# Performance work log

Hardware: AMD Instinct MI355X
Metric: run time of the kernel (lower is better)

Reference implementation:

```python
import jax, jax.numpy as jnp
import numpy as np

HEADS = 32
DK = 32            # att_size = hidden // heads
CUT = 15.5         # tot_dis[cur_layer=0] + 0.5
NEG = -1e8
LN_EPS = 1e-5


def layernorm(x, g, b):
    m = jnp.mean(x, axis=-1, keepdims=True)
    v = jnp.mean((x - m) ** 2, axis=-1, keepdims=True)
    return (x - m) / jnp.sqrt(v + LN_EPS) * g + b


def setup_inputs() -> dict:
    key = jax.random.key(0)
    ks = jax.random.split(key, 12)
    B, S, H, F = 8, 513, 1024, 4096
    N = S - 1
    def nrm(k, shape, scale=0.02):
        return jax.random.normal(k, shape, jnp.float32) * scale
    x = jax.random.normal(ks[0], (B, S, H), jnp.float32)
    attn_bias = jax.random.normal(ks[1], (B, HEADS, S, S), jnp.float32)
    rel_pos = jax.random.randint(ks[2], (B, N, N), 0, 16, jnp.int32)
    rel_emb = nrm(ks[3], (512, HEADS)).at[0].set(0.0)  # padding_idx=0
    Wq = nrm(ks[4], (H, H)); bq = jnp.zeros((H,), jnp.float32)
    Wk = nrm(ks[5], (H, H)); bk = jnp.zeros((H,), jnp.float32)
    Wv = nrm(ks[6], (H, H)); bv = jnp.zeros((H,), jnp.float32)
    Wo = nrm(ks[7], (H, H)); bo = jnp.zeros((H,), jnp.float32)
    W1 = nrm(ks[8], (H, F)); b1 = jnp.zeros((F,), jnp.float32)
    W2 = nrm(ks[9], (F, H)); b2 = jnp.zeros((H,), jnp.float32)
    ln1_g = jnp.ones((H,), jnp.float32); ln1_b = jnp.zeros((H,), jnp.float32)
    ln2_g = jnp.ones((H,), jnp.float32); ln2_b = jnp.zeros((H,), jnp.float32)
    return dict(x=x, attn_bias=attn_bias, rel_emb=rel_emb,
                Wq=Wq, bq=bq, Wk=Wk, bk=bk, Wv=Wv, bv=bv, Wo=Wo, bo=bo,
                W1=W1, b1=b1, W2=W2, b2=b2,
                ln1_g=ln1_g, ln1_b=ln1_b, ln2_g=ln2_g, ln2_b=ln2_b,
                rel_pos=rel_pos)


def reference(x, attn_bias, rel_emb, Wq, bq, Wk, bk, Wv, bv, Wo, bo,
              W1, b1, W2, b2, ln1_g, ln1_b, ln2_g, ln2_b, rel_pos):
    B, S, H = x.shape
    # rel-pos bias: embed [B,N,N] -> [B,N,N,heads] -> [B,heads,N,N]
    rpb = jnp.transpose(rel_emb[rel_pos], (0, 3, 1, 2))
    inner = attn_bias[:, :, 1:, 1:] + rpb
    # per-head mask flag: keep if within cutoff distance OR already -inf-masked
    flags = (rel_pos[:, None, :, :] <= CUT) | (inner < NEG)
    ab = attn_bias.at[:, :, 1:, 1:].set(inner * flags)
    # attention
    y = layernorm(x, ln1_g, ln1_b)
    scale = DK ** -0.5
    q = (y @ Wq + bq).reshape(B, S, HEADS, DK) * scale
    k = (y @ Wk + bk).reshape(B, S, HEADS, DK)
    v = (y @ Wv + bv).reshape(B, S, HEADS, DK)
    scores = jnp.einsum('bqhd,bkhd->bhqk', q, k) + ab
    attn = jax.nn.softmax(scores, axis=-1)
    o = jnp.einsum('bhqk,bkhd->bqhd', attn, v).reshape(B, S, H)
    x = x + (o @ Wo + bo)
    # FFN
    y = layernorm(x, ln2_g, ln2_b)
    y = jax.nn.gelu(y @ W1 + b1, approximate=False) @ W2 + b2
    return x + y
```

## Files before the change

kernel.cpp:

```cpp
#include <hip/hip_runtime.h>
#include <hip/hip_bf16.h>
#include <math.h>

typedef __attribute__((ext_vector_type(8))) short short8;
typedef __attribute__((ext_vector_type(4))) float f32x4;
typedef unsigned short u16;
typedef unsigned int u32;

#define SQ 513
#define MPAD 4224
#define MV 4104
#define NHEADS 32
#define DKH 32

static __device__ inline u16 f2bf(float f) {
  u32 u = __builtin_bit_cast(u32, f);
  u = (u + 0x7fffu + ((u >> 16) & 1u)) >> 16;
  return (u16)u;
}

static __device__ inline void gld16(const void* g, void* l) {
  __builtin_amdgcn_global_load_lds((__attribute__((address_space(1))) void*)g,
                                   (__attribute__((address_space(3))) void*)l,
                                   16, 0, 0);
}

static __device__ inline float gelu_f(float x) {
  return 0.5f * x * (1.f + erff(x * 0.70710678118654752f));
}

__global__ __launch_bounds__(256) void transpose_cast_k(const float* __restrict__ in,
    u16* __restrict__ out, int K, int N, float scale)
{
  __shared__ float t[32][33];
  int n0 = blockIdx.x * 32, k0 = blockIdx.y * 32;
  int tx = threadIdx.x & 31, ty = threadIdx.x >> 5;
#pragma unroll
  for (int i = 0; i < 32; i += 8)
    t[ty + i][tx] = in[(size_t)(k0 + ty + i) * N + n0 + tx];
  __syncthreads();
#pragma unroll
  for (int i = 0; i < 32; i += 8)
    out[(size_t)(n0 + ty + i) * K + k0 + tx] = f2bf(t[tx][ty + i] * scale);
}

__global__ __launch_bounds__(256) void prep_bias_k(const float* __restrict__ bq,
    const float* __restrict__ bk, const float* __restrict__ bv,
    float* __restrict__ out, float scale)
{
  int i = blockIdx.x * 256 + threadIdx.x;
  float v = (i < 1024) ? bq[i] * scale : ((i < 2048) ? bk[i - 1024] : bv[i - 2048]);
  out[i] = v;
}

__global__ __launch_bounds__(256) void ln_k(const float* __restrict__ in,
    const float* __restrict__ g, const float* __restrict__ b,
    u16* __restrict__ out)
{
  int row = blockIdx.x;
  float4 v = ((const float4*)(in + (size_t)row * 1024))[threadIdx.x];
  float s = v.x + v.y + v.z + v.w;
  float s2 = v.x * v.x + v.y * v.y + v.z * v.z + v.w * v.w;
#pragma unroll
  for (int d = 32; d; d >>= 1) { s += __shfl_xor(s, d, 64); s2 += __shfl_xor(s2, d, 64); }
  __shared__ float ps[4], ps2[4];
  int w = threadIdx.x >> 6;
  if ((threadIdx.x & 63) == 0) { ps[w] = s; ps2[w] = s2; }
  __syncthreads();
  s = ps[0] + ps[1] + ps[2] + ps[3];
  s2 = ps2[0] + ps2[1] + ps2[2] + ps2[3];
  float mean = s * (1.f / 1024.f);
  float var = s2 * (1.f / 1024.f) - mean * mean;
  float inv = rsqrtf(var + 1e-5f);
  float4 gv = ((const float4*)g)[threadIdx.x];
  float4 bv = ((const float4*)b)[threadIdx.x];
  ushort4 o;
  o.x = f2bf((v.x - mean) * inv * gv.x + bv.x);
  o.y = f2bf((v.y - mean) * inv * gv.y + bv.y);
  o.z = f2bf((v.z - mean) * inv * gv.z + bv.z);
  o.w = f2bf((v.w - mean) * inv * gv.w + bv.w);
  ((ushort4*)(out + (size_t)row * 1024))[threadIdx.x] = o;
}

template <int EPI>
__global__ __launch_bounds__(256) void gemm_bt(const u16* __restrict__ A,
    const u16* __restrict__ Bw, const float* __restrict__ bias,
    const float* __restrict__ resid, void* __restrict__ outp,
    int N, int K, int nbx)
{
  __shared__ alignas(16) u16 sA[128 * 64];
  __shared__ alignas(16) u16 sB[128 * 64];
  int tid = threadIdx.x;
  int l = tid & 63, lg = l >> 4, li = l & 15;
  int mb = blockIdx.x / nbx, nb = blockIdx.x % nbx;
  int m0 = mb * 128, n0 = nb * 128;
  int wv = tid >> 6;
  int wr = wv >> 1, wc = wv & 1;
  f32x4 acc[4][4] = {};
  int r_ = tid >> 3, c_ = (tid & 7) * 8;
  const u16* Ag = A + (size_t)(m0 + r_) * K + c_;
  const u16* Bg = Bw + (size_t)(n0 + r_) * K + c_;
  u16* sAb = sA + (tid & 192) * 8;
  u16* sBb = sB + (tid & 192) * 8;

  for (int k0 = 0; k0 < K; k0 += 64) {
    __syncthreads();
#pragma unroll
    for (int i = 0; i < 4; ++i) {
      gld16(Ag + (size_t)(i * 32) * K + k0, sAb + i * 2048);
      gld16(Bg + (size_t)(i * 32) * K + k0, sBb + i * 2048);
    }
    __syncthreads();
#pragma unroll
    for (int ks = 0; ks < 2; ++ks) {
      short8 af[4], bfr[4];
#pragma unroll
      for (int i = 0; i < 4; ++i)
        af[i] = *(const short8*)&sA[(64 * wr + 16 * i + li) * 64 + ks * 32 + lg * 8];
#pragma unroll
      for (int j = 0; j < 4; ++j)
        bfr[j] = *(const short8*)&sB[(64 * wc + 16 * j + li) * 64 + ks * 32 + lg * 8];
#pragma unroll
      for (int i = 0; i < 4; ++i)
#pragma unroll
        for (int j = 0; j < 4; ++j)
          acc[i][j] = __builtin_amdgcn_mfma_f32_16x16x32_bf16(af[i], bfr[j], acc[i][j], 0, 0, 0);
    }
  }

#pragma unroll
  for (int i = 0; i < 4; ++i) {
    int rb = m0 + 64 * wr + 16 * i + 4 * lg;
#pragma unroll
    for (int j = 0; j < 4; ++j) {
      int col = n0 + 64 * wc + 16 * j + li;
      float bia = bias[col];
#pragma unroll
      for (int r = 0; r < 4; ++r) {
        int row = rb + r;
        float v = acc[i][j][r] + bia;
        if (EPI == 0) {
          ((u16*)outp)[(size_t)row * N + col] = f2bf(v);
        } else if (EPI == 1) {
          if (row < MV) {
            v += resid[(size_t)row * N + col];
            ((float*)outp)[(size_t)row * N + col] = v;
          }
        } else if (EPI == 2) {
          ((u16*)outp)[(size_t)row * N + col] = f2bf(gelu_f(v));
        } else {
          if (row < MV) ((float*)outp)[(size_t)row * N + col] += v;
        }
      }
    }
  }
}

__global__ __launch_bounds__(256) void attn_fused(const u16* __restrict__ qkv,
    const float* __restrict__ attn_bias, const int* __restrict__ rel_pos,
    const float* __restrict__ rel_emb, u16* __restrict__ o)
{
  __shared__ alignas(16) u16 k_lds[64][40];
  __shared__ alignas(16) u16 vT_lds[32][72];
  __shared__ alignas(16) u16 p_lds[4][16][72];
  int bid = blockIdx.x;
  int qt = bid % 9, h = (bid / 9) % NHEADS, b = bid / (9 * NHEADS);
  int tid = threadIdx.x, wv = tid >> 6, l = tid & 63, lg = l >> 4, li = l & 15;
  int q0 = qt * 64;

  short8 qfrag = *(const short8*)(qkv + (size_t)(b * SQ + q0 + 16 * wv + li) * 3072 + h * DKH + lg * 8);

  float tv = rel_emb[(size_t)(l & 15) * NHEADS + h];

  int sqb = q0 + 16 * wv + 4 * lg;
  const float* bias_row[4];
  const int* rp_row[4];
#pragma unroll
  for (int r = 0; r < 4; ++r) {
    int sq = sqb + r;
    int sqc = sq > 512 ? 512 : sq;
    bias_row[r] = attn_bias + (((size_t)b * NHEADS + h) * SQ + sqc) * SQ;
    int sqm = sq - 1; sqm = sqm < 0 ? 0 : (sqm > 511 ? 511 : sqm);
    rp_row[r] = rel_pos + ((size_t)b * 512 + sqm) * 512;
  }

  int kr = tid >> 2, kc = (tid & 3) * 8;
  const u16* kbase = qkv + 1024 + h * DKH + kc;
  const u16* vbase = qkv + 2048 + h * DKH + kc;

  float pb[4][4];
  int pr[4][4];
  short8 kreg, vreg;

  {
    int sk0 = kr;
    int srow = b * SQ + sk0;
    kreg = *(const short8*)(kbase + (size_t)srow * 3072);
    vreg = *(const short8*)(vbase + (size_t)srow * 3072);
#pragma unroll
    for (int f = 0; f < 4; ++f) {
      int sk = 16 * f + li;
      int skm = sk - 1; skm = skm < 0 ? 0 : skm;
#pragma unroll
      for (int r = 0; r < 4; ++r) {
        pb[f][r] = bias_row[r][sk];
        pr[f][r] = rp_row[r][skm];
      }
    }
  }

  f32x4 o_acc[2] = {};
  float m_run[4], l_run[4];
#pragma unroll
  for (int r = 0; r < 4; ++r) { m_run[r] = -1e30f; l_run[r] = 0.f; }

  for (int kt = 0; kt < 9; ++kt) {
    __syncthreads();
    *(short8*)&k_lds[kr][kc] = kreg;
#pragma unroll
    for (int e = 0; e < 8; ++e) vT_lds[kc + e][kr] = (u16)vreg[e];
    __syncthreads();

    f32x4 sc[4];
#pragma unroll
    for (int f = 0; f < 4; ++f) {
      short8 kf = *(const short8*)&k_lds[16 * f + li][lg * 8];
      f32x4 z = {};
      sc[f] = __builtin_amdgcn_mfma_f32_16x16x32_bf16(qfrag, kf, z, 0, 0, 0);
    }

#pragma unroll
    for (int f = 0; f < 4; ++f) {
      int sk = kt * 64 + 16 * f + li;
#pragma unroll
      for (int r = 0; r < 4; ++r) {
        int sq = sqb + r;
        float base = pb[f][r];
        int rp = pr[f][r];
        float re = __shfl(tv, rp, 64);
        float inner = base + re;
        float ab = (rp <= 15 || inner < -1e8f) ? inner : 0.f;
        if (sq == 0 || sk == 0) ab = base;
        if (sq > 512 || sk > 512) ab = -1e30f;
        sc[f][r] += ab;
      }
    }

    if (kt < 8) {
      int skn = (kt + 1) * 64 + kr;
      int srow = b * SQ + (skn > 512 ? 512 : skn);
      kreg = *(const short8*)(kbase + (size_t)srow * 3072);
      vreg = *(const short8*)(vbase + (size_t)srow * 3072);
#pragma unroll
      for (int f = 0; f < 4; ++f) {
        int sk = (kt + 1) * 64 + 16 * f + li;
        int skc = sk > 512 ? 512 : sk;
        int skm = sk - 1; skm = skm > 511 ? 511 : skm;
#pragma unroll
        for (int r = 0; r < 4; ++r) {
          pb[f][r] = bias_row[r][skc];
          pr[f][r] = rp_row[r][skm];
        }
      }
    }

    float alpha[4];
#pragma unroll
    for (int r = 0; r < 4; ++r) {
      float mx = fmaxf(fmaxf(sc[0][r], sc[1][r]), fmaxf(sc[2][r], sc[3][r]));
#pragma unroll
      for (int d = 1; d < 16; d <<= 1) mx = fmaxf(mx, __shfl_xor(mx, d, 16));
      float mn = fmaxf(m_run[r], mx);
      alpha[r] = __expf(m_run[r] - mn);
      m_run[r] = mn;
      l_run[r] *= alpha[r];
    }
#pragma unroll
    for (int f = 0; f < 4; ++f)
#pragma unroll
      for (int r = 0; r < 4; ++r) {
        float p = __expf(sc[f][r] - m_run[r]);
        l_run[r] += p;
        p_lds[wv][4 * lg + r][16 * f + li] = f2bf(p);
      }
#pragma unroll
    for (int df = 0; df < 2; ++df)
#pragma unroll
      for (int r = 0; r < 4; ++r) o_acc[df][r] *= alpha[r];

#pragma unroll
    for (int kk = 0; kk < 2; ++kk) {
      short8 pa = *(const short8*)&p_lds[wv][li][kk * 32 + lg * 8];
#pragma unroll
      for (int df = 0; df < 2; ++df) {
        short8 vb = *(const short8*)&vT_lds[16 * df + li][kk * 32 + lg * 8];
        o_acc[df] = __builtin_amdgcn_mfma_f32_16x16x32_bf16(pa, vb, o_acc[df], 0, 0, 0);
      }
    }
  }

#pragma unroll
  for (int r = 0; r < 4; ++r) {
    float s = l_run[r];
#pragma unroll
    for (int d = 1; d < 16; d <<= 1) s += __shfl_xor(s, d, 16);
    l_run[r] = s;
  }
#pragma unroll
  for (int df = 0; df < 2; ++df)
#pragma unroll
    for (int r = 0; r < 4; ++r) {
      int s_q = sqb + r;
      if (s_q <= 512)
        o[(size_t)(b * SQ + s_q) * 1024 + h * DKH + 16 * df + li] = f2bf(o_acc[df][r] / l_run[r]);
    }
}

extern "C" void kernel_launch(void* const* d_in, const int* in_sizes, int n_in,
                              void* d_out, int out_size, void* d_ws, size_t ws_size,
                              hipStream_t stream) {
  const float* x        = (const float*)d_in[0];
  const float* attn_bias= (const float*)d_in[1];
  const float* rel_emb  = (const float*)d_in[2];
  const float* Wq = (const float*)d_in[3];
  const float* bq = (const float*)d_in[4];
  const float* Wk = (const float*)d_in[5];
  const float* bk = (const float*)d_in[6];
  const float* Wv = (const float*)d_in[7];
  const float* bv = (const float*)d_in[8];
  const float* Wo = (const float*)d_in[9];
  const float* bo = (const float*)d_in[10];
  const float* W1 = (const float*)d_in[11];
  const float* b1 = (const float*)d_in[12];
  const float* W2 = (const float*)d_in[13];
  const float* b2 = (const float*)d_in[14];
  const float* ln1g = (const float*)d_in[15];
  const float* ln1b = (const float*)d_in[16];
  const float* ln2g = (const float*)d_in[17];
  const float* ln2b = (const float*)d_in[18];
  const int*   rel_pos = (const int*)d_in[19];
  float* out = (float*)d_out;

  char* ws = (char*)d_ws;
  size_t off = 0;
  auto alloc = [&](size_t bytes) { char* p = ws + off; off += (bytes + 255) & ~(size_t)255; return p; };
  u16* w_qkvT = (u16*)alloc((size_t)3072 * 1024 * 2);
  u16* w_oT   = (u16*)alloc((size_t)1024 * 1024 * 2);
  u16* w_1T   = (u16*)alloc((size_t)4096 * 1024 * 2);
  u16* w_2T   = (u16*)alloc((size_t)1024 * 4096 * 2);
  float* bias_qkv = (float*)alloc(3072 * 4);
  u16* ybuf = (u16*)alloc((size_t)MPAD * 1024 * 2);
  u16* obuf = (u16*)alloc((size_t)MPAD * 1024 * 2);
  u16* big  = (u16*)alloc((size_t)MPAD * 4096 * 2);

  const float scale = 0.17677669529663689f;
  dim3 blk(256);

  transpose_cast_k<<<dim3(32, 32), blk, 0, stream>>>(Wq, w_qkvT, 1024, 1024, scale);
  transpose_cast_k<<<dim3(32, 32), blk, 0, stream>>>(Wk, w_qkvT + (size_t)1024 * 1024, 1024, 1024, 1.f);
  transpose_cast_k<<<dim3(32, 32), blk, 0, stream>>>(Wv, w_qkvT + (size_t)2048 * 1024, 1024, 1024, 1.f);
  transpose_cast_k<<<dim3(32, 32), blk, 0, stream>>>(Wo, w_oT, 1024, 1024, 1.f);
  transpose_cast_k<<<dim3(128, 32), blk, 0, stream>>>(W1, w_1T, 1024, 4096, 1.f);
  transpose_cast_k<<<dim3(32, 128), blk, 0, stream>>>(W2, w_2T, 4096, 1024, 1.f);
  prep_bias_k<<<12, blk, 0, stream>>>(bq, bk, bv, bias_qkv, scale);

  ln_k<<<MV, blk, 0, stream>>>(x, ln1g, ln1b, ybuf);
  gemm_bt<0><<<33 * 24, blk, 0, stream>>>(ybuf, w_qkvT, bias_qkv, nullptr, big, 3072, 1024, 24);
  attn_fused<<<8 * NHEADS * 9, blk, 0, stream>>>(big, attn_bias, rel_pos, rel_emb, obuf);
  gemm_bt<1><<<33 * 8, blk, 0, stream>>>(obuf, w_oT, bo, x, out, 1024, 1024, 8);
  ln_k<<<MV, blk, 0, stream>>>(out, ln2g, ln2b, ybuf);
  gemm_bt<2><<<33 * 32, blk, 0, stream>>>(ybuf, w_1T, b1, nullptr, big, 4096, 1024, 32);
  gemm_bt<3><<<33 * 8, blk, 0, stream>>>(big, w_2T, b2, nullptr, out, 1024, 4096, 8);
}
```

Baseline: 500.5 us.

## Pre-transpose V and load attention K/V fragments directly from global memory

Adds a small kernel that writes V per batch and head in a transposed, padded layout. The attention kernel then loads K and V MFMA fragments straight from global memory into registers and prefetches the next tile's fragments, instead of staging them through LDS. This removes the per-tile LDS stores, the scattered transposing LDS writes and two block barriers per key tile. In exchange it adds an extra launch, a V-sized buffer round trip, and uncoalesced strided K reads.

```diff
diff --git a/kernel.cpp b/kernel.cpp
--- a/kernel.cpp
+++ b/kernel.cpp
@@ -12,6 +12,7 @@
 #define MV 4104
 #define NHEADS 32
 #define DKH 32
+#define SVP 576
 
 static __device__ inline u16 f2bf(float f) {
   u32 u = __builtin_bit_cast(u32, f);
@@ -42,6 +43,26 @@
 #pragma unroll
   for (int i = 0; i < 32; i += 8)
     out[(size_t)(n0 + ty + i) * K + k0 + tx] = f2bf(t[tx][ty + i] * scale);
+}
+
+__global__ __launch_bounds__(256) void vtrans_k(const u16* __restrict__ qkv,
+    u16* __restrict__ vT)
+{
+  __shared__ u16 t[32][33];
+  int st = blockIdx.x * 32, h = blockIdx.y, b = blockIdx.z;
+  int tx = threadIdx.x & 31, ty = threadIdx.x >> 5;
+#pragma unroll
+  for (int i = 0; i < 32; i += 8) {
+    int s = st + ty + i;
+    int sc = s > 512 ? 512 : s;
+    t[ty + i][tx] = qkv[(size_t)(b * SQ + sc) * 3072 + 2048 + h * DKH + tx];
+  }
+  __syncthreads();
+#pragma unroll
+  for (int i = 0; i < 32; i += 8) {
+    int d = ty + i;
+    vT[(((size_t)b * NHEADS + h) * DKH + d) * SVP + st + tx] = t[tx][d];
+  }
 }
 
 __global__ __launch_bounds__(256) void prep_bias_k(const float* __restrict__ bq,
@@ -157,22 +178,21 @@
 }
 
 __global__ __launch_bounds__(256) void attn_fused(const u16* __restrict__ qkv,
-    const float* __restrict__ attn_bias, const int* __restrict__ rel_pos,
-    const float* __restrict__ rel_emb, u16* __restrict__ o)
-{
-  __shared__ alignas(16) u16 k_lds[64][40];
-  __shared__ alignas(16) u16 vT_lds[32][72];
+    const u16* __restrict__ vT, const float* __restrict__ attn_bias,
+    const int* __restrict__ rel_pos, const float* __restrict__ rel_emb,
+    u16* __restrict__ o)
+{
   __shared__ alignas(16) u16 p_lds[4][16][72];
   int bid = blockIdx.x;
   int qt = bid % 9, h = (bid / 9) % NHEADS, b = bid / (9 * NHEADS);
   int tid = threadIdx.x, wv = tid >> 6, l = tid & 63, lg = l >> 4, li = l & 15;
   int q0 = qt * 64;
+  int sqb = q0 + 16 * wv + 4 * lg;
 
   short8 qfrag = *(const short8*)(qkv + (size_t)(b * SQ + q0 + 16 * wv + li) * 3072 + h * DKH + lg * 8);
 
-  float tv = rel_emb[(size_t)(l & 15) * NHEADS + h];
-
-  int sqb = q0 + 16 * wv + 4 * lg;
+  float tv = rel_emb[(size_t)li * NHEADS + h];
+
   const float* bias_row[4];
   const int* rp_row[4];
 #pragma unroll
@@ -184,28 +204,29 @@
     rp_row[r] = rel_pos + ((size_t)b * 512 + sqm) * 512;
   }
 
-  int kr = tid >> 2, kc = (tid & 3) * 8;
-  const u16* kbase = qkv + 1024 + h * DKH + kc;
-  const u16* vbase = qkv + 2048 + h * DKH + kc;
-
+  const u16* kfb = qkv + (size_t)(b * SQ) * 3072 + 1024 + h * DKH + lg * 8;
+  const u16* vtb = vT + (((size_t)b * NHEADS + h) * DKH) * SVP + lg * 8;
+
+  short8 kf[4], vb[4];
   float pb[4][4];
   int pr[4][4];
-  short8 kreg, vreg;
-
-  {
-    int sk0 = kr;
-    int srow = b * SQ + sk0;
-    kreg = *(const short8*)(kbase + (size_t)srow * 3072);
-    vreg = *(const short8*)(vbase + (size_t)srow * 3072);
-#pragma unroll
-    for (int f = 0; f < 4; ++f) {
-      int sk = 16 * f + li;
-      int skm = sk - 1; skm = skm < 0 ? 0 : skm;
-#pragma unroll
-      for (int r = 0; r < 4; ++r) {
-        pb[f][r] = bias_row[r][sk];
-        pr[f][r] = rp_row[r][skm];
-      }
+
+#pragma unroll
+  for (int f = 0; f < 4; ++f)
+    kf[f] = *(const short8*)(kfb + (size_t)(16 * f + li) * 3072);
+#pragma unroll
+  for (int u = 0; u < 4; ++u) {
+    int df = u >> 1, kk = u & 1;
+    vb[u] = *(const short8*)(vtb + (size_t)(16 * df + li) * SVP + kk * 32);
+  }
+#pragma unroll
+  for (int f = 0; f < 4; ++f) {
+    int sk = 16 * f + li;
+    int skm = sk - 1; skm = skm < 0 ? 0 : skm;
+#pragma unroll
+    for (int r = 0; r < 4; ++r) {
+      pb[f][r] = bias_row[r][sk];
+      pr[f][r] = rp_row[r][skm];
     }
   }
 
@@ -215,18 +236,17 @@
   for (int r = 0; r < 4; ++r) { m_run[r] = -1e30f; l_run[r] = 0.f; }
 
   for (int kt = 0; kt < 9; ++kt) {
-    __syncthreads();
-    *(short8*)&k_lds[kr][kc] = kreg;
-#pragma unroll
-    for (int e = 0; e < 8; ++e) vT_lds[kc + e][kr] = (u16)vreg[e];
-    __syncthreads();
-
     f32x4 sc[4];
 #pragma unroll
     for (int f = 0; f < 4; ++f) {
-      short8 kf = *(const short8*)&k_lds[16 * f + li][lg * 8];
       f32x4 z = {};
-      sc[f] = __builtin_amdgcn_mfma_f32_16x16x32_bf16(qfrag, kf, z, 0, 0, 0);
+      sc[f] = __builtin_amdgcn_mfma_f32_16x16x32_bf16(qfrag, kf[f], z, 0, 0, 0);
+    }
+    if (kt < 8) {
+      const u16* kfn = kfb + (size_t)((kt + 1) * 64) * 3072;
+#pragma unroll
+      for (int f = 0; f < 4; ++f)
+        kf[f] = *(const short8*)(kfn + (size_t)(16 * f + li) * 3072);
     }
 
 #pragma unroll
@@ -245,12 +265,7 @@
         sc[f][r] += ab;
       }
     }
-
     if (kt < 8) {
-      int skn = (kt + 1) * 64 + kr;
-      int srow = b * SQ + (skn > 512 ? 512 : skn);
-      kreg = *(const short8*)(kbase + (size_t)srow * 3072);
-      vreg = *(const short8*)(vbase + (size_t)srow * 3072);
 #pragma unroll
       for (int f = 0; f < 4; ++f) {
         int sk = (kt + 1) * 64 + 16 * f + li;
@@ -292,9 +307,15 @@
     for (int kk = 0; kk < 2; ++kk) {
       short8 pa = *(const short8*)&p_lds[wv][li][kk * 32 + lg * 8];
 #pragma unroll
-      for (int df = 0; df < 2; ++df) {
-        short8 vb = *(const short8*)&vT_lds[16 * df + li][kk * 32 + lg * 8];
-        o_acc[df] = __builtin_amdgcn_mfma_f32_16x16x32_bf16(pa, vb, o_acc[df], 0, 0, 0);
+      for (int df = 0; df < 2; ++df)
+        o_acc[df] = __builtin_amdgcn_mfma_f32_16x16x32_bf16(pa, vb[df * 2 + kk], o_acc[df], 0, 0, 0);
+    }
+    if (kt < 8) {
+      const u16* vtn = vtb + (kt + 1) * 64;
+#pragma unroll
+      for (int u = 0; u < 4; ++u) {
+        int df = u >> 1, kk = u & 1;
+        vb[u] = *(const short8*)(vtn + (size_t)(16 * df + li) * SVP + kk * 32);
       }
     }
   }
@@ -351,6 +372,7 @@
   float* bias_qkv = (float*)alloc(3072 * 4);
   u16* ybuf = (u16*)alloc((size_t)MPAD * 1024 * 2);
   u16* obuf = (u16*)alloc((size_t)MPAD * 1024 * 2);
+  u16* vTb  = (u16*)alloc((size_t)8 * NHEADS * DKH * SVP * 2);
   u16* big  = (u16*)alloc((size_t)MPAD * 4096 * 2);
 
   const float scale = 0.17677669529663689f;
@@ -366,7 +388,8 @@
 
   ln_k<<<MV, blk, 0, stream>>>(x, ln1g, ln1b, ybuf);
   gemm_bt<0><<<33 * 24, blk, 0, stream>>>(ybuf, w_qkvT, bias_qkv, nullptr, big, 3072, 1024, 24);
-  attn_fused<<<8 * NHEADS * 9, blk, 0, stream>>>(big, attn_bias, rel_pos, rel_emb, obuf);
+  vtrans_k<<<dim3(18, NHEADS, 8), blk, 0, stream>>>(big, vTb);
+  attn_fused<<<8 * NHEADS * 9, blk, 0, stream>>>(big, vTb, attn_bias, rel_pos, rel_emb, obuf);
   gemm_bt<1><<<33 * 8, blk, 0, stream>>>(obuf, w_oT, bo, x, out, 1024, 1024, 8);
   ln_k<<<MV, blk, 0, stream>>>(out, ln2g, ln2b, ybuf);
   gemm_bt<2><<<33 * 32, blk, 0, stream>>>(ybuf, w_1T, b1, nullptr, big, 4096, 1024, 32);
```

Result: slower. 549.0 us (+9.7%).
